# Kernel tuning notes

Hardware: AMD Instinct MI355X
Metric: run time of the kernel (lower is better)

## Reference

```python
import jax, jax.numpy as jnp
import numpy as np

# Blade metric for Cl(1,3) inner product <~A B>_0: sign per basis blade =
# (-1)^{k(k-1)/2} * prod(eta_ii) with eta = diag(1,-1,-1,-1).
# Order: 1 | e0 e1 e2 e3 | e01 e02 e03 e12 e13 e23 | e012 e013 e023 e123 | e0123
BLADE_METRIC = jnp.array(
    [1.0,
     1.0, -1.0, -1.0, -1.0,
     1.0, 1.0, 1.0, -1.0, -1.0, -1.0,
     -1.0, -1.0, -1.0, 1.0,
     -1.0],
    dtype=jnp.float32,
)

B, H, N, MVC, SC = 8, 8, 1024, 8, 32


def setup_inputs() -> dict:
    key = jax.random.key(0)
    ks = jax.random.split(key, 6)
    mv_shape = (B, H, N, MVC, 16)
    s_shape = (B, H, N, SC)
    return {
        "q_mv": jax.random.normal(ks[0], mv_shape, dtype=jnp.float32),
        "k_mv": jax.random.normal(ks[1], mv_shape, dtype=jnp.float32),
        "v_mv": jax.random.normal(ks[2], mv_shape, dtype=jnp.float32),
        "q_s": jax.random.normal(ks[3], s_shape, dtype=jnp.float32),
        "k_s": jax.random.normal(ks[4], s_shape, dtype=jnp.float32),
        "v_s": jax.random.normal(ks[5], s_shape, dtype=jnp.float32),
    }


def reference(q_mv, k_mv, v_mv, q_s, k_s, v_s):
    *lead, n_out, mvc, _ = q_mv.shape
    n_in = k_mv.shape[-3]
    sc = q_s.shape[-1]
    d = 16 * mvc + sc  # total feature dim used for the softmax scale

    # Apply GA blade metric to queries, flatten mv channels, concat scalars.
    qf = jnp.concatenate(
        [(q_mv * BLADE_METRIC).reshape(*lead, n_out, mvc * 16), q_s], axis=-1
    )
    kf = jnp.concatenate([k_mv.reshape(*lead, n_in, mvc * 16), k_s], axis=-1)
    vf = jnp.concatenate([v_mv.reshape(*lead, n_in, mvc * 16), v_s], axis=-1)

    scores = jnp.einsum("bhid,bhjd->bhij", qf, kf) / jnp.sqrt(
        jnp.asarray(d, dtype=qf.dtype)
    )
    attn = jax.nn.softmax(scores, axis=-1)
    out = jnp.einsum("bhij,bhjd->bhid", attn, vf)

    out_mv = out[..., : mvc * 16].reshape(*lead, n_out, mvc, 16)
    out_s = out[..., mvc * 16 :]
    return out_mv, out_s
```

## Files before the change

### kernel.cpp

```cpp
#include <hip/hip_runtime.h>

typedef __attribute__((ext_vector_type(8))) _Float16 f16x8;
typedef __attribute__((ext_vector_type(4))) float f32x4;

#define BHn 64
#define Nn 1024

static constexpr int kOutMvElems = 8 * 8 * 1024 * 128;
static constexpr float kScaleLog2e = 0.11405506f;
static constexpr unsigned kNegMask = 0xBF1Cu;
static constexpr int kBlob = 20480;

typedef __attribute__((address_space(1))) const void* gas1_t;
typedef __attribute__((address_space(3))) void* las3_t;
__device__ __forceinline__ void dma16(const _Float16* g, _Float16* l) {
  __builtin_amdgcn_global_load_lds((gas1_t)g, (las3_t)l, 16, 0, 0);
}
__device__ __forceinline__ float fast_exp2(float x) {
  float r;
  asm("v_exp_f32 %0, %1" : "=v"(r) : "v"(x));
  return r;
}

__global__ __launch_bounds__(256) void pack_kernel(const float* __restrict__ kmv,
                                                   const float* __restrict__ ks,
                                                   const float* __restrict__ vmv,
                                                   const float* __restrict__ vs,
                                                   _Float16* __restrict__ KV) {
  __shared__ _Float16 tk[64][184];
  __shared__ _Float16 tv[160][72];
  const int kt = blockIdx.x;
  const int bh = blockIdx.y;
  const int tid = threadIdx.x;
#pragma unroll
  for (int i = 0; i < 5; ++i) {
    int s = tid + 256 * i;
    int key = s / 20, p = s - key * 20;
    int row = bh * Nn + kt * 64 + key;
    const float* src = (p < 16) ? (kmv + (size_t)row * 128 + p * 8)
                                : (ks + (size_t)row * 32 + (p - 16) * 8);
    float4 a = *(const float4*)src;
    float4 b = *(const float4*)(src + 4);
    f16x8 h;
    h[0] = (_Float16)a.x; h[1] = (_Float16)a.y; h[2] = (_Float16)a.z; h[3] = (_Float16)a.w;
    h[4] = (_Float16)b.x; h[5] = (_Float16)b.y; h[6] = (_Float16)b.z; h[7] = (_Float16)b.w;
    *(f16x8*)&tk[key][p * 8] = h;
  }
  for (int s = tid; s < 64 * 40; s += 256) {
    int key = s / 40, p = s - key * 40;
    int row = bh * Nn + kt * 64 + key;
    const float* src = (p < 32) ? (vmv + (size_t)row * 128 + p * 4)
                                : (vs + (size_t)row * 32 + (p - 32) * 4);
    float4 v = *(const float4*)src;
    int d = p * 4;
    tv[d + 0][key] = (_Float16)v.x;
    tv[d + 1][key] = (_Float16)v.y;
    tv[d + 2][key] = (_Float16)v.z;
    tv[d + 3][key] = (_Float16)v.w;
  }
  __syncthreads();
  _Float16* dst = KV + ((size_t)bh * 16 + kt) * kBlob;
#pragma unroll
  for (int i = 0; i < 5; ++i) {
    int u = tid + 256 * i;
    int p = u >> 6, key = u & 63;
    f16x8 h = *(const f16x8*)&tk[key][p * 8];
    *(f16x8*)&dst[p * 512 + key * 8] = h;
  }
#pragma unroll
  for (int i = 0; i < 5; ++i) {
    int u = tid + 256 * i;
    int s = u / 160, d = u - s * 160;
    int c32 = (s >> 2) * 32, gg = s & 3;
    f16x8 h;
#pragma unroll
    for (int i2 = 0; i2 < 8; ++i2) {
      int key = c32 + ((i2 < 4) ? (gg * 4 + i2) : (16 + gg * 4 + (i2 - 4)));
      h[i2] = tv[d][key];
    }
    *(f16x8*)&dst[10240 + u * 8] = h;
  }
}

__global__ __launch_bounds__(512, 1) void geo_attn_kernel(const float* __restrict__ qmv,
                                                          const float* __restrict__ qs,
                                                          const _Float16* __restrict__ KV,
                                                          float* __restrict__ out) {
  __shared__ __align__(16) _Float16 kv[3 * kBlob];

  const int b = blockIdx.x;
  const int sw = (b & 7) * 32 + (b >> 3);
  const int qb = sw & 3;
  const int bh = sw >> 2;

  const int tid = threadIdx.x;
  const int w = tid >> 6;
  const int l = tid & 63;
  const int g = l >> 4;
  const int nn = l & 15;

  const _Float16* blob0 = KV + (size_t)bh * 16 * kBlob;

  int kbase[5];
#pragma unroll
  for (int c = 0; c < 5; ++c) kbase[c] = (4 * c + g) * 512 + nn * 8;
  int vbase[2];
#pragma unroll
  for (int ch = 0; ch < 2; ++ch) vbase[ch] = 10240 + (4 * ch + g) * 1280 + nn * 8;

  f16x8 qf[2][5];
#pragma unroll
  for (int q2 = 0; q2 < 2; ++q2) {
    const size_t qbase = (size_t)(bh * Nn + qb * 256 + w * 32 + q2 * 16 + nn);
#pragma unroll
    for (int c = 0; c < 5; ++c) {
      const float* src = (c < 4) ? (qmv + qbase * 128 + c * 32 + 8 * g)
                                 : (qs + qbase * 32 + 8 * g);
      float4 a = *(const float4*)src;
      float4 bb = *(const float4*)(src + 4);
      float x[8] = {a.x, a.y, a.z, a.w, bb.x, bb.y, bb.z, bb.w};
#pragma unroll
      for (int i = 0; i < 8; ++i) {
        float v = x[i] * kScaleLog2e;
        if (c < 4) {
          int idx = ((g & 1) << 3) + i;
          v = ((kNegMask >> idx) & 1u) ? -v : v;
        }
        qf[q2][c][i] = (_Float16)v;
      }
    }
  }

  f32x4 acc[2][10];
#pragma unroll
  for (int q2 = 0; q2 < 2; ++q2)
#pragma unroll
    for (int j = 0; j < 10; ++j) acc[q2][j] = (f32x4){0.f, 0.f, 0.f, 0.f};
  float Ma = 12.f, Mb = 12.f, La = 0.f, Lb = 0.f;

  f32x4 sa[4], sb[4];
  f16x8 paf[2], pbf[2];

  const int laneOff = l * 8 + w * 512;
  auto stage = [&](int t, int buf) {
    const _Float16* src = blob0 + (size_t)t * kBlob + laneOff;
    _Float16* dst = &kv[buf * kBlob + w * 512];
#pragma unroll
    for (int i = 0; i < 5; ++i) dma16(src + i * 4096, dst + i * 4096);
  };

  auto do_qk = [&](const _Float16* blob) {
#pragma unroll
    for (int kb = 0; kb < 4; ++kb) {
      sa[kb] = (f32x4){0.f, 0.f, 0.f, 0.f};
      sb[kb] = (f32x4){0.f, 0.f, 0.f, 0.f};
    }
    f16x8 kf[5][4];
#pragma unroll
    for (int c = 0; c < 2; ++c)
#pragma unroll
      for (int kb = 0; kb < 4; ++kb) kf[c][kb] = *(const f16x8*)&blob[kbase[c] + kb * 128];
#pragma unroll
    for (int c = 0; c < 5; ++c) {
      if (c + 2 < 5) {
#pragma unroll
        for (int kb = 0; kb < 4; ++kb)
          kf[c + 2][kb] = *(const f16x8*)&blob[kbase[c + 2] + kb * 128];
      }
#pragma unroll
      for (int kb = 0; kb < 4; ++kb) {
        sa[kb] = __builtin_amdgcn_mfma_f32_16x16x32_f16(kf[c][kb], qf[0][c], sa[kb], 0, 0, 0);
        sb[kb] = __builtin_amdgcn_mfma_f32_16x16x32_f16(kf[c][kb], qf[1][c], sb[kb], 0, 0, 0);
      }
    }
  };
  auto do_pv = [&](const _Float16* blob) {
    f16x8 vf[4];
#pragma unroll
    for (int i = 0; i < 4; ++i)
      vf[i] = *(const f16x8*)&blob[vbase[i / 10] + (i % 10) * 128];
#pragma unroll
    for (int i = 0; i < 20; ++i) {
      f16x8 cu = vf[i & 3];
      if (i + 4 < 20)
        vf[i & 3] = *(const f16x8*)&blob[vbase[(i + 4) / 10] + ((i + 4) % 10) * 128];
      const int ch = i / 10, j = i % 10;
      acc[0][j] = __builtin_amdgcn_mfma_f32_16x16x32_f16(paf[ch], cu, acc[0][j], 0, 0, 0);
      acc[1][j] = __builtin_amdgcn_mfma_f32_16x16x32_f16(pbf[ch], cu, acc[1][j], 0, 0, 0);
    }
  };
  auto do_softmax = [&]() {
    float rsa = 0.f, rsb = 0.f;
#pragma unroll
    for (int kb = 0; kb < 4; ++kb) {
      const int ch = kb >> 1, off = (kb & 1) * 4;
#pragma unroll
      for (int r = 0; r < 4; ++r) {
        float pa_ = fast_exp2(sa[kb][r] - Ma);
        float pb_ = fast_exp2(sb[kb][r] - Mb);
        rsa += pa_; rsb += pb_;
        paf[ch][off + r] = (_Float16)pa_;
        pbf[ch][off + r] = (_Float16)pb_;
      }
    }
    if (__builtin_expect(__any((int)(rsa > 3.2e4f || rsb > 3.2e4f)), 0)) {
      float lma = sa[0][0], lmb = sb[0][0];
#pragma unroll
      for (int kb = 0; kb < 4; ++kb)
#pragma unroll
        for (int r = 0; r < 4; ++r) {
          lma = fmaxf(lma, sa[kb][r]);
          lmb = fmaxf(lmb, sb[kb][r]);
        }
      lma = fmaxf(lma, __shfl_xor(lma, 16)); lma = fmaxf(lma, __shfl_xor(lma, 32));
      lmb = fmaxf(lmb, __shfl_xor(lmb, 16)); lmb = fmaxf(lmb, __shfl_xor(lmb, 32));
      float nMa = fmaxf(Ma, lma); float fsa = fast_exp2(Ma - nMa); Ma = nMa;
      float nMb = fmaxf(Mb, lmb); float fsb = fast_exp2(Mb - nMb); Mb = nMb;
      La *= fsa; Lb *= fsb;
      float fa[4], fb[4];
#pragma unroll
      for (int r = 0; r < 4; ++r) {
        fa[r] = __shfl(fsa, 4 * g + r, 16);
        fb[r] = __shfl(fsb, 4 * g + r, 16);
      }
#pragma unroll
      for (int j = 0; j < 10; ++j)
#pragma unroll
        for (int r = 0; r < 4; ++r) {
          acc[0][j][r] *= fa[r];
          acc[1][j][r] *= fb[r];
        }
      rsa = 0.f; rsb = 0.f;
#pragma unroll
      for (int kb = 0; kb < 4; ++kb) {
        const int ch = kb >> 1, off = (kb & 1) * 4;
#pragma unroll
        for (int r = 0; r < 4; ++r) {
          float pa_ = fast_exp2(sa[kb][r] - Ma);
          float pb_ = fast_exp2(sb[kb][r] - Mb);
          rsa += pa_; rsb += pb_;
          paf[ch][off + r] = (_Float16)pa_;
          pbf[ch][off + r] = (_Float16)pb_;
        }
      }
    }
    La += rsa;
    Lb += rsb;
  };

  stage(0, 0);
  stage(1, 1);

  for (int t = 0; t < 16; ++t) {
    if (t == 15) asm volatile("s_waitcnt vmcnt(0)" ::: "memory");
    else         asm volatile("s_waitcnt vmcnt(5)" ::: "memory");
    __builtin_amdgcn_s_barrier();
    __builtin_amdgcn_sched_barrier(0);
    if (t + 2 < 16) stage(t + 2, (t + 2) % 3);
    const _Float16* blob = &kv[(t % 3) * kBlob];
    __builtin_amdgcn_s_setprio(1);
    do_qk(blob);
    __builtin_amdgcn_s_setprio(0);
    do_softmax();
    __builtin_amdgcn_s_setprio(1);
    do_pv(blob);
    __builtin_amdgcn_s_setprio(0);
  }

  La += __shfl_xor(La, 16); La += __shfl_xor(La, 32);
  Lb += __shfl_xor(Lb, 16); Lb += __shfl_xor(Lb, 32);
  float ria = 1.f / La, rib = 1.f / Lb;
  float ra[4], rb_[4];
#pragma unroll
  for (int r = 0; r < 4; ++r) {
    ra[r] = __shfl(ria, 4 * g + r, 16);
    rb_[r] = __shfl(rib, 4 * g + r, 16);
  }
  const int row0 = bh * Nn + qb * 256 + w * 32;
#pragma unroll
  for (int j = 0; j < 10; ++j) {
    const int d = 16 * j + nn;
#pragma unroll
    for (int r = 0; r < 4; ++r) {
      float v0 = acc[0][j][r] * ra[r];
      float v1 = acc[1][j][r] * rb_[r];
      const int r0 = row0 + 4 * g + r;
      const int r1 = row0 + 16 + 4 * g + r;
      if (d < 128) {
        out[(size_t)r0 * 128 + d] = v0;
        out[(size_t)r1 * 128 + d] = v1;
      } else {
        out[(size_t)kOutMvElems + (size_t)r0 * 32 + (d - 128)] = v0;
        out[(size_t)kOutMvElems + (size_t)r1 * 32 + (d - 128)] = v1;
      }
    }
  }
}

extern "C" void kernel_launch(void* const* d_in, const int* in_sizes, int n_in,
                              void* d_out, int out_size, void* d_ws, size_t ws_size,
                              hipStream_t stream) {
  const float* qmv = (const float*)d_in[0];
  const float* kmv = (const float*)d_in[1];
  const float* vmv = (const float*)d_in[2];
  const float* qs = (const float*)d_in[3];
  const float* ks = (const float*)d_in[4];
  const float* vs = (const float*)d_in[5];
  float* out = (float*)d_out;

  _Float16* KV = (_Float16*)d_ws;

  pack_kernel<<<dim3(16, BHn), dim3(256), 0, stream>>>(kmv, ks, vmv, vs, KV);
  geo_attn_kernel<<<dim3(256), dim3(512), 0, stream>>>(qmv, qs, KV, out);
}
```

Measured before the change: 77.98 us.

## Switch attention MFMAs from 16x16x32 to 32x32x16 tiles with repacked V layout

Each wave now handles its 32 query rows with 32x32x16 f16 MFMAs instead of pairs of 16x16x32 MFMAs. The pack kernel reorders V so each lane's fragment matches the new accumulator layout. The softmax, rescale and output indexing are rewritten for the 16-register accumulator. The aim is fewer MFMA issues, fewer LDS fragment loads and less per-row bookkeeping, in exchange for a different register footprint and the risk of layout mistakes.

```diff
diff --git a/kernel.cpp b/kernel.cpp
--- a/kernel.cpp
+++ b/kernel.cpp
@@ -1,7 +1,7 @@
 #include <hip/hip_runtime.h>
 
 typedef __attribute__((ext_vector_type(8))) _Float16 f16x8;
-typedef __attribute__((ext_vector_type(4))) float f32x4;
+typedef __attribute__((ext_vector_type(16))) float f32x16;
 
 #define BHn 64
 #define Nn 1024
@@ -70,14 +70,16 @@
 #pragma unroll
   for (int i = 0; i < 5; ++i) {
     int u = tid + 256 * i;
-    int s = u / 160, d = u - s * 160;
-    int c32 = (s >> 2) * 32, gg = s & 3;
+    int dcol = u & 31;
+    int rest = u >> 5;
+    int dt = rest % 5;
+    int s8 = rest / 5;
+    int kb = (s8 >> 1) * 16 + (s8 & 1) * 4;
+    int d = 32 * dt + dcol;
     f16x8 h;
 #pragma unroll
-    for (int i2 = 0; i2 < 8; ++i2) {
-      int key = c32 + ((i2 < 4) ? (gg * 4 + i2) : (16 + gg * 4 + (i2 - 4)));
-      h[i2] = tv[d][key];
-    }
+    for (int i2 = 0; i2 < 8; ++i2)
+      h[i2] = tv[d][kb + (i2 & 3) + ((i2 >> 2) << 3)];
     *(f16x8*)&dst[10240 + u * 8] = h;
   }
 }
@@ -96,50 +98,44 @@
   const int tid = threadIdx.x;
   const int w = tid >> 6;
   const int l = tid & 63;
-  const int g = l >> 4;
-  const int nn = l & 15;
+  const int h = l >> 5;
+  const int dcol = l & 31;
 
   const _Float16* blob0 = KV + (size_t)bh * 16 * kBlob;
 
-  int kbase[5];
-#pragma unroll
-  for (int c = 0; c < 5; ++c) kbase[c] = (4 * c + g) * 512 + nn * 8;
-  int vbase[2];
-#pragma unroll
-  for (int ch = 0; ch < 2; ++ch) vbase[ch] = 10240 + (4 * ch + g) * 1280 + nn * 8;
-
-  f16x8 qf[2][5];
-#pragma unroll
-  for (int q2 = 0; q2 < 2; ++q2) {
-    const size_t qbase = (size_t)(bh * Nn + qb * 256 + w * 32 + q2 * 16 + nn);
-#pragma unroll
-    for (int c = 0; c < 5; ++c) {
-      const float* src = (c < 4) ? (qmv + qbase * 128 + c * 32 + 8 * g)
-                                 : (qs + qbase * 32 + 8 * g);
-      float4 a = *(const float4*)src;
-      float4 bb = *(const float4*)(src + 4);
-      float x[8] = {a.x, a.y, a.z, a.w, bb.x, bb.y, bb.z, bb.w};
-#pragma unroll
-      for (int i = 0; i < 8; ++i) {
-        float v = x[i] * kScaleLog2e;
-        if (c < 4) {
-          int idx = ((g & 1) << 3) + i;
-          v = ((kNegMask >> idx) & 1u) ? -v : v;
-        }
-        qf[q2][c][i] = (_Float16)v;
-      }
-    }
-  }
-
-  f32x4 acc[2][10];
-#pragma unroll
-  for (int q2 = 0; q2 < 2; ++q2)
-#pragma unroll
-    for (int j = 0; j < 10; ++j) acc[q2][j] = (f32x4){0.f, 0.f, 0.f, 0.f};
-  float Ma = 12.f, Mb = 12.f, La = 0.f, Lb = 0.f;
-
-  f32x4 sa[4], sb[4];
-  f16x8 paf[2], pbf[2];
+  const int kb0 = h * 512 + dcol * 8;
+  const int vb0 = 10240 + h * 1280 + dcol * 8;
+
+  const int row0w = bh * Nn + qb * 256 + w * 32;
+  const size_t qrow = (size_t)(row0w + dcol);
+  f16x8 qf2[10];
+#pragma unroll
+  for (int c = 0; c < 10; ++c) {
+    const float* src = (c < 8) ? (qmv + qrow * 128 + c * 16 + 8 * h)
+                               : (qs + qrow * 32 + (c - 8) * 16 + 8 * h);
+    float4 a = *(const float4*)src;
+    float4 b4 = *(const float4*)(src + 4);
+    float x[8] = {a.x, a.y, a.z, a.w, b4.x, b4.y, b4.z, b4.w};
+#pragma unroll
+    for (int i = 0; i < 8; ++i) {
+      float v = x[i] * kScaleLog2e;
+      if (c < 8) {
+        int idx = 8 * h + i;
+        v = ((kNegMask >> idx) & 1u) ? -v : v;
+      }
+      qf2[c][i] = (_Float16)v;
+    }
+  }
+
+  f32x16 acc2[5];
+#pragma unroll
+  for (int dt = 0; dt < 5; ++dt)
+#pragma unroll
+    for (int r = 0; r < 16; ++r) acc2[dt][r] = 0.f;
+  float Ma = 12.f, La = 0.f;
+
+  f32x16 s2[2];
+  f16x8 pfr[4];
 
   const int laneOff = l * 8 + w * 512;
   auto stage = [&](int t, int buf) {
@@ -151,101 +147,77 @@
 
   auto do_qk = [&](const _Float16* blob) {
 #pragma unroll
-    for (int kb = 0; kb < 4; ++kb) {
-      sa[kb] = (f32x4){0.f, 0.f, 0.f, 0.f};
-      sb[kb] = (f32x4){0.f, 0.f, 0.f, 0.f};
-    }
-    f16x8 kf[5][4];
+    for (int r = 0; r < 16; ++r) { s2[0][r] = 0.f; s2[1][r] = 0.f; }
+    f16x8 kw[3][2];
 #pragma unroll
     for (int c = 0; c < 2; ++c)
 #pragma unroll
-      for (int kb = 0; kb < 4; ++kb) kf[c][kb] = *(const f16x8*)&blob[kbase[c] + kb * 128];
-#pragma unroll
-    for (int c = 0; c < 5; ++c) {
-      if (c + 2 < 5) {
-#pragma unroll
-        for (int kb = 0; kb < 4; ++kb)
-          kf[c + 2][kb] = *(const f16x8*)&blob[kbase[c + 2] + kb * 128];
-      }
-#pragma unroll
-      for (int kb = 0; kb < 4; ++kb) {
-        sa[kb] = __builtin_amdgcn_mfma_f32_16x16x32_f16(kf[c][kb], qf[0][c], sa[kb], 0, 0, 0);
-        sb[kb] = __builtin_amdgcn_mfma_f32_16x16x32_f16(kf[c][kb], qf[1][c], sb[kb], 0, 0, 0);
-      }
+      for (int kt = 0; kt < 2; ++kt)
+        kw[c][kt] = *(const f16x8*)&blob[kb0 + c * 1024 + kt * 256];
+#pragma unroll
+    for (int c = 0; c < 10; ++c) {
+      if (c + 2 < 10) {
+#pragma unroll
+        for (int kt = 0; kt < 2; ++kt)
+          kw[(c + 2) % 3][kt] = *(const f16x8*)&blob[kb0 + (c + 2) * 1024 + kt * 256];
+      }
+      s2[0] = __builtin_amdgcn_mfma_f32_32x32x16_f16(kw[c % 3][0], qf2[c], s2[0], 0, 0, 0);
+      s2[1] = __builtin_amdgcn_mfma_f32_32x32x16_f16(kw[c % 3][1], qf2[c], s2[1], 0, 0, 0);
     }
   };
   auto do_pv = [&](const _Float16* blob) {
     f16x8 vf[4];
 #pragma unroll
     for (int i = 0; i < 4; ++i)
-      vf[i] = *(const f16x8*)&blob[vbase[i / 10] + (i % 10) * 128];
+      vf[i] = *(const f16x8*)&blob[vb0 + (i / 5) * 2560 + (i % 5) * 256];
 #pragma unroll
     for (int i = 0; i < 20; ++i) {
       f16x8 cu = vf[i & 3];
       if (i + 4 < 20)
-        vf[i & 3] = *(const f16x8*)&blob[vbase[(i + 4) / 10] + ((i + 4) % 10) * 128];
-      const int ch = i / 10, j = i % 10;
-      acc[0][j] = __builtin_amdgcn_mfma_f32_16x16x32_f16(paf[ch], cu, acc[0][j], 0, 0, 0);
-      acc[1][j] = __builtin_amdgcn_mfma_f32_16x16x32_f16(pbf[ch], cu, acc[1][j], 0, 0, 0);
+        vf[i & 3] = *(const f16x8*)&blob[vb0 + ((i + 4) / 5) * 2560 + ((i + 4) % 5) * 256];
+      const int kc = i / 5, dt = i % 5;
+      acc2[dt] = __builtin_amdgcn_mfma_f32_32x32x16_f16(pfr[kc], cu, acc2[dt], 0, 0, 0);
     }
   };
   auto do_softmax = [&]() {
-    float rsa = 0.f, rsb = 0.f;
-#pragma unroll
-    for (int kb = 0; kb < 4; ++kb) {
-      const int ch = kb >> 1, off = (kb & 1) * 4;
-#pragma unroll
-      for (int r = 0; r < 4; ++r) {
-        float pa_ = fast_exp2(sa[kb][r] - Ma);
-        float pb_ = fast_exp2(sb[kb][r] - Mb);
-        rsa += pa_; rsb += pb_;
-        paf[ch][off + r] = (_Float16)pa_;
-        pbf[ch][off + r] = (_Float16)pb_;
-      }
-    }
-    if (__builtin_expect(__any((int)(rsa > 3.2e4f || rsb > 3.2e4f)), 0)) {
-      float lma = sa[0][0], lmb = sb[0][0];
-#pragma unroll
-      for (int kb = 0; kb < 4; ++kb)
-#pragma unroll
-        for (int r = 0; r < 4; ++r) {
-          lma = fmaxf(lma, sa[kb][r]);
-          lmb = fmaxf(lmb, sb[kb][r]);
+    float rs = 0.f;
+#pragma unroll
+    for (int kt = 0; kt < 2; ++kt)
+#pragma unroll
+      for (int r = 0; r < 16; ++r) {
+        float p_ = fast_exp2(s2[kt][r] - Ma);
+        rs += p_;
+        pfr[2 * kt + (r >> 3)][r & 7] = (_Float16)p_;
+      }
+    if (__builtin_expect(__any((int)(rs > 3.2e4f)), 0)) {
+      float lm = s2[0][0];
+#pragma unroll
+      for (int kt = 0; kt < 2; ++kt)
+#pragma unroll
+        for (int r = 0; r < 16; ++r) lm = fmaxf(lm, s2[kt][r]);
+      lm = fmaxf(lm, __shfl_xor(lm, 32));
+      float nM = fmaxf(Ma, lm);
+      float fs = fast_exp2(Ma - nM);
+      Ma = nM;
+      La *= fs;
+#pragma unroll
+      for (int r = 0; r < 16; ++r) {
+        int q = (r & 3) + 8 * (r >> 2) + 4 * h;
+        float fr = __shfl(fs, q, 32);
+#pragma unroll
+        for (int dt = 0; dt < 5; ++dt) acc2[dt][r] *= fr;
+      }
+      rs = 0.f;
+#pragma unroll
+      for (int kt = 0; kt < 2; ++kt)
+#pragma unroll
+        for (int r = 0; r < 16; ++r) {
+          float p_ = fast_exp2(s2[kt][r] - Ma);
+          rs += p_;
+          pfr[2 * kt + (r >> 3)][r & 7] = (_Float16)p_;
         }
-      lma = fmaxf(lma, __shfl_xor(lma, 16)); lma = fmaxf(lma, __shfl_xor(lma, 32));
-      lmb = fmaxf(lmb, __shfl_xor(lmb, 16)); lmb = fmaxf(lmb, __shfl_xor(lmb, 32));
-      float nMa = fmaxf(Ma, lma); float fsa = fast_exp2(Ma - nMa); Ma = nMa;
-      float nMb = fmaxf(Mb, lmb); float fsb = fast_exp2(Mb - nMb); Mb = nMb;
-      La *= fsa; Lb *= fsb;
-      float fa[4], fb[4];
-#pragma unroll
-      for (int r = 0; r < 4; ++r) {
-        fa[r] = __shfl(fsa, 4 * g + r, 16);
-        fb[r] = __shfl(fsb, 4 * g + r, 16);
-      }
-#pragma unroll
-      for (int j = 0; j < 10; ++j)
-#pragma unroll
-        for (int r = 0; r < 4; ++r) {
-          acc[0][j][r] *= fa[r];
-          acc[1][j][r] *= fb[r];
-        }
-      rsa = 0.f; rsb = 0.f;
-#pragma unroll
-      for (int kb = 0; kb < 4; ++kb) {
-        const int ch = kb >> 1, off = (kb & 1) * 4;
-#pragma unroll
-        for (int r = 0; r < 4; ++r) {
-          float pa_ = fast_exp2(sa[kb][r] - Ma);
-          float pb_ = fast_exp2(sb[kb][r] - Mb);
-          rsa += pa_; rsb += pb_;
-          paf[ch][off + r] = (_Float16)pa_;
-          pbf[ch][off + r] = (_Float16)pb_;
-        }
-      }
-    }
-    La += rsa;
-    Lb += rsb;
+    }
+    La += rs;
   };
 
   stage(0, 0);
@@ -267,32 +239,20 @@
     __builtin_amdgcn_s_setprio(0);
   }
 
-  La += __shfl_xor(La, 16); La += __shfl_xor(La, 32);
-  Lb += __shfl_xor(Lb, 16); Lb += __shfl_xor(Lb, 32);
-  float ria = 1.f / La, rib = 1.f / Lb;
-  float ra[4], rb_[4];
-#pragma unroll
-  for (int r = 0; r < 4; ++r) {
-    ra[r] = __shfl(ria, 4 * g + r, 16);
-    rb_[r] = __shfl(rib, 4 * g + r, 16);
-  }
-  const int row0 = bh * Nn + qb * 256 + w * 32;
-#pragma unroll
-  for (int j = 0; j < 10; ++j) {
-    const int d = 16 * j + nn;
-#pragma unroll
-    for (int r = 0; r < 4; ++r) {
-      float v0 = acc[0][j][r] * ra[r];
-      float v1 = acc[1][j][r] * rb_[r];
-      const int r0 = row0 + 4 * g + r;
-      const int r1 = row0 + 16 + 4 * g + r;
-      if (d < 128) {
-        out[(size_t)r0 * 128 + d] = v0;
-        out[(size_t)r1 * 128 + d] = v1;
-      } else {
-        out[(size_t)kOutMvElems + (size_t)r0 * 32 + (d - 128)] = v0;
-        out[(size_t)kOutMvElems + (size_t)r1 * 32 + (d - 128)] = v1;
-      }
+  La += __shfl_xor(La, 32);
+  float ri = 1.f / La;
+#pragma unroll
+  for (int r = 0; r < 16; ++r) {
+    const int q = (r & 3) + 8 * (r >> 2) + 4 * h;
+    float ra = __shfl(ri, q, 32);
+    const size_t orow = (size_t)(row0w + q);
+#pragma unroll
+    for (int dt = 0; dt < 5; ++dt) {
+      float v = acc2[dt][r] * ra;
+      if (dt < 4)
+        out[orow * 128 + 32 * dt + dcol] = v;
+      else
+        out[(size_t)kOutMvElems + orow * 32 + dcol] = v;
     }
   }
 }
```

Measured after the change: 78.36 us. No clear change (+0.5%).
